# Optimization experiments

Hardware: AMD Instinct MI355X
Metric: run time of the kernel (lower is better)

Reference implementation:

```python
import jax, jax.numpy as jnp
import numpy as np

B, NQ, NK = 8, 1024, 1024
DQ = DK = DV = 512
H = 8
DH = DV // H
EPS = 1e-5
NEG = -1e9


def _layer_norm(x, g, b):
    mu = jnp.mean(x, axis=-1, keepdims=True)
    var = jnp.mean(jnp.square(x - mu), axis=-1, keepdims=True)
    return (x - mu) * jax.lax.rsqrt(var + EPS) * g + b


def setup_inputs() -> dict:
    key = jax.random.key(0)
    ks = jax.random.split(key, 16)
    s_q = 1.0 / np.sqrt(DQ)
    s_k = 1.0 / np.sqrt(DK)
    s_v = 1.0 / np.sqrt(DV)
    return {
        "Q": jax.random.normal(ks[0], (B, NQ, DQ), jnp.float32),
        "K": jax.random.normal(ks[1], (B, NK, DK), jnp.float32),
        "mask": jax.random.randint(ks[2], (B, NK), 0, 2, jnp.int32),
        "Wq": jax.random.uniform(ks[3], (DQ, DV), jnp.float32, -s_q, s_q),
        "bq": jax.random.uniform(ks[4], (DV,), jnp.float32, -s_q, s_q),
        "Wk": jax.random.uniform(ks[5], (DK, DV), jnp.float32, -s_k, s_k),
        "bk": jax.random.uniform(ks[6], (DV,), jnp.float32, -s_k, s_k),
        "Wv": jax.random.uniform(ks[7], (DK, DV), jnp.float32, -s_k, s_k),
        "bv": jax.random.uniform(ks[8], (DV,), jnp.float32, -s_k, s_k),
        "Wo": jax.random.uniform(ks[9], (DV, DV), jnp.float32, -s_v, s_v),
        "bo": jax.random.uniform(ks[10], (DV,), jnp.float32, -s_v, s_v),
        "g0": jnp.ones((DV,), jnp.float32),
        "b0": jnp.zeros((DV,), jnp.float32),
        "g1": jnp.ones((DV,), jnp.float32),
        "b1": jnp.zeros((DV,), jnp.float32),
    }


def reference(Q, K, mask, Wq, bq, Wk, bk, Wv, bv, Wo, bo, g0, b0, g1, b1):
    b = Q.shape[0]
    # projections: [B, N, DV] -> [B, N, H, DH]
    q = (Q @ Wq + bq).reshape(b, -1, H, DH)
    k = (K @ Wk + bk).reshape(b, -1, H, DH)
    v = (K @ Wv + bv).reshape(b, -1, H, DH)
    scores = jnp.einsum("bqhd,bkhd->bhqk", q, k) / np.sqrt(DH)  # [B,H,Nq,Nk]
    scores = jnp.where((mask == 0)[:, None, None, :], NEG, scores)
    A = jax.nn.softmax(scores, axis=-1)
    o = q + jnp.einsum("bhqk,bkhd->bqhd", A, v)  # residual on projected Q (per head)
    O = o.reshape(b, -1, DV)
    O = _layer_norm(O, g0, b0)
    O = O + jax.nn.relu(O @ Wo + bo)
    O = _layer_norm(O, g1, b1)
    return O
```

## Files before the change

### kernel.cpp

```cpp
#include <hip/hip_runtime.h>


typedef float f32x4 __attribute__((ext_vector_type(4)));
typedef short bf16x8 __attribute__((ext_vector_type(8)));
typedef unsigned short u16;

#define MFMA16 __builtin_amdgcn_mfma_f32_16x16x32_bf16

__device__ __forceinline__ float bf2f(u16 u){
    unsigned x = ((unsigned)u) << 16;
    return __builtin_bit_cast(float, x);
}
__device__ __forceinline__ u16 f2bf(float f){
    unsigned u = __builtin_bit_cast(unsigned, f);
    u = u + 0x7fffu + ((u >> 16) & 1u);
    return (u16)(u >> 16);
}

__global__ __launch_bounds__(256) void transpose_w(
    const float* __restrict__ Wq, const float* __restrict__ Wk,
    const float* __restrict__ Wv, const float* __restrict__ Wo,
    u16* __restrict__ wt)
{
    const int z = blockIdx.z;
    const float* W = (z == 0) ? Wq : (z == 1) ? Wk : (z == 2) ? Wv : Wo;
    u16* out = wt + (size_t)z * 512 * 512;

    __shared__ u16 tile[32][33];
    const int k0 = blockIdx.y * 32, n0 = blockIdx.x * 32;
    const int c = threadIdx.x & 31, r = threadIdx.x >> 5;
#pragma unroll
    for (int i = 0; i < 4; i++) {
        int rr = r + i * 8;
        tile[rr][c] = f2bf(W[(size_t)(k0 + rr) * 512 + n0 + c]);
    }
    __syncthreads();
#pragma unroll
    for (int i = 0; i < 4; i++) {
        int rr = r + i * 8;
        out[(size_t)(n0 + rr) * 512 + k0 + c] = tile[c][rr];
    }
}

__global__ __launch_bounds__(256) void transpose_v(
    const u16* __restrict__ vb, u16* __restrict__ vtg)
{
    __shared__ u16 tile[32][33];
    const int bh = blockIdx.z;
    const int b = bh >> 3, h = bh & 7;
    const int k0 = blockIdx.x * 32, d0 = blockIdx.y * 32;
    const int c = threadIdx.x & 31, r = threadIdx.x >> 5;
#pragma unroll
    for (int i = 0; i < 4; i++) {
        int rr = r + i * 8;
        tile[rr][c] = vb[(size_t)(b * 1024 + k0 + rr) * 512 + h * 64 + d0 + c];
    }
    __syncthreads();
#pragma unroll
    for (int i = 0; i < 4; i++) {
        int rr = r + i * 8;
        vtg[(size_t)(bh * 64 + d0 + rr) * 1024 + k0 + c] = tile[c][rr];
    }
}

__global__ __launch_bounds__(256) void gemm_proj(
    const float* __restrict__ Q, const float* __restrict__ K,
    const u16* __restrict__ wt,
    const float* __restrict__ bq, const float* __restrict__ bk, const float* __restrict__ bv,
    u16* __restrict__ qb, u16* __restrict__ kb, u16* __restrict__ vb)
{
    __shared__ __align__(16) u16 lds_a[128 * 40];
    __shared__ __align__(16) u16 lds_b[128 * 40];

    const int z = blockIdx.z;
    const float* X = (z == 0) ? Q : K;
    const u16* Wt = wt + (size_t)z * 512 * 512;
    const float* bias = (z == 0) ? bq : (z == 1) ? bk : bv;
    u16* outb = (z == 0) ? qb : (z == 1) ? kb : vb;

    const int bm = blockIdx.y, bn = blockIdx.x;
    const int t = threadIdx.x;
    const int wave = t >> 6, lane = t & 63, quad = lane >> 4, lm = lane & 15;
    const int wm = wave >> 1, wn = wave & 1;

    f32x4 acc[4][4];
    const f32x4 zz = {0.f, 0.f, 0.f, 0.f};
#pragma unroll
    for (int i = 0; i < 4; i++)
#pragma unroll
        for (int j = 0; j < 4; j++) acc[i][j] = zz;

    for (int k0 = 0; k0 < 512; k0 += 32) {
#pragma unroll
        for (int i = 0; i < 2; i++) {
            int idx = t + i * 256;
            int r = idx >> 2, c = (idx & 3) * 8;
            const float* xp = &X[(size_t)(bm * 128 + r) * 512 + k0 + c];
            f32x4 a0 = *(const f32x4*)xp;
            f32x4 a1 = *(const f32x4*)(xp + 4);
            bf16x8 xv;
#pragma unroll
            for (int j = 0; j < 4; j++) { xv[j] = (short)f2bf(a0[j]); xv[4 + j] = (short)f2bf(a1[j]); }
            *(bf16x8*)&lds_a[r * 40 + c] = xv;
            *(bf16x8*)&lds_b[r * 40 + c] =
                *(const bf16x8*)&Wt[(size_t)(bn * 128 + r) * 512 + k0 + c];
        }
        __syncthreads();
        bf16x8 af[4], bfr[4];
#pragma unroll
        for (int mi = 0; mi < 4; mi++)
            af[mi] = *(const bf16x8*)&lds_a[(wm * 64 + mi * 16 + lm) * 40 + quad * 8];
#pragma unroll
        for (int ni = 0; ni < 4; ni++)
            bfr[ni] = *(const bf16x8*)&lds_b[(wn * 64 + ni * 16 + lm) * 40 + quad * 8];
#pragma unroll
        for (int mi = 0; mi < 4; mi++)
#pragma unroll
            for (int ni = 0; ni < 4; ni++)
                acc[mi][ni] = MFMA16(af[mi], bfr[ni], acc[mi][ni], 0, 0, 0);
        __syncthreads();
    }

#pragma unroll
    for (int mi = 0; mi < 4; mi++) {
#pragma unroll
        for (int ni = 0; ni < 4; ni++) {
            const int col = bn * 128 + wn * 64 + ni * 16 + lm;
            const float bv_ = bias[col];
#pragma unroll
            for (int r = 0; r < 4; r++) {
                const int row = bm * 128 + wm * 64 + mi * 16 + quad * 4 + r;
                outb[(size_t)row * 512 + col] = f2bf(acc[mi][ni][r] + bv_);
            }
        }
    }
}

__global__ __launch_bounds__(256) void gemm_mlp(
    const u16* __restrict__ X, const u16* __restrict__ wt,
    const float* __restrict__ bo, const float* __restrict__ resid,
    float* __restrict__ outf)
{
    __shared__ __align__(16) u16 lds_a[128 * 40];
    __shared__ __align__(16) u16 lds_b[128 * 40];

    const u16* Wt = wt + (size_t)3 * 512 * 512;
    const int bm = blockIdx.y, bn = blockIdx.x;
    const int t = threadIdx.x;
    const int wave = t >> 6, lane = t & 63, quad = lane >> 4, lm = lane & 15;
    const int wm = wave >> 1, wn = wave & 1;

    f32x4 acc[4][4];
    const f32x4 zz = {0.f, 0.f, 0.f, 0.f};
#pragma unroll
    for (int i = 0; i < 4; i++)
#pragma unroll
        for (int j = 0; j < 4; j++) acc[i][j] = zz;

    for (int k0 = 0; k0 < 512; k0 += 32) {
#pragma unroll
        for (int i = 0; i < 2; i++) {
            int idx = t + i * 256;
            int r = idx >> 2, c = (idx & 3) * 8;
            *(bf16x8*)&lds_a[r * 40 + c] =
                *(const bf16x8*)&X[(size_t)(bm * 128 + r) * 512 + k0 + c];
            *(bf16x8*)&lds_b[r * 40 + c] =
                *(const bf16x8*)&Wt[(size_t)(bn * 128 + r) * 512 + k0 + c];
        }
        __syncthreads();
        bf16x8 af[4], bfr[4];
#pragma unroll
        for (int mi = 0; mi < 4; mi++)
            af[mi] = *(const bf16x8*)&lds_a[(wm * 64 + mi * 16 + lm) * 40 + quad * 8];
#pragma unroll
        for (int ni = 0; ni < 4; ni++)
            bfr[ni] = *(const bf16x8*)&lds_b[(wn * 64 + ni * 16 + lm) * 40 + quad * 8];
#pragma unroll
        for (int mi = 0; mi < 4; mi++)
#pragma unroll
            for (int ni = 0; ni < 4; ni++)
                acc[mi][ni] = MFMA16(af[mi], bfr[ni], acc[mi][ni], 0, 0, 0);
        __syncthreads();
    }

#pragma unroll
    for (int mi = 0; mi < 4; mi++) {
#pragma unroll
        for (int ni = 0; ni < 4; ni++) {
            const int col = bn * 128 + wn * 64 + ni * 16 + lm;
            const float bv_ = bo[col];
#pragma unroll
            for (int r = 0; r < 4; r++) {
                const int row = bm * 128 + wm * 64 + mi * 16 + quad * 4 + r;
                const size_t off = (size_t)row * 512 + col;
                outf[off] = resid[off] + fmaxf(acc[mi][ni][r] + bv_, 0.f);
            }
        }
    }
}

__global__ __launch_bounds__(256) void attn_kernel(
    const u16* __restrict__ qb, const u16* __restrict__ kb, const u16* __restrict__ vtg,
    const int* __restrict__ mask, float* __restrict__ O)
{
    __shared__ __align__(16) u16 k_tile[64 * 88];
    __shared__ __align__(16) u16 vt[64 * 88];
    __shared__ __align__(16) u16 p_st[4 * 32 * 88];
    __shared__ float mskf[1024];

    const int i = blockIdx.x;
    const int s_ = i >> 3;
    const int bh = (i & 7) + 8 * (s_ >> 3);
    const int qt = s_ & 7;
    const int b = bh >> 3, h = bh & 7;

    const int t = threadIdx.x, wave = t >> 6, lane = t & 63;
    const int quad = lane >> 4, lm = lane & 15;
    const int qbase = qt * 128 + wave * 32;
    const size_t baseb = (size_t)b * 1024 * 512;
    const size_t vbase = (size_t)((b * 8 + h) * 64) * 1024;

#pragma unroll
    for (int ii = 0; ii < 4; ii++) {
        int j = t + ii * 256;
        mskf[j] = mask[b * 1024 + j] ? 1.0f : 0.0f;
    }

    bf16x8 aq[2][2];
#pragma unroll
    for (int m = 0; m < 2; m++)
#pragma unroll
        for (int ks = 0; ks < 2; ks++)
            aq[m][ks] = *(const bf16x8*)&qb[baseb +
                (size_t)(qbase + m * 16 + lm) * 512 + h * 64 + ks * 32 + quad * 8];

    float lsum[2][4];
    f32x4 oacc[2][4];
    const f32x4 zz = {0.f, 0.f, 0.f, 0.f};
#pragma unroll
    for (int m = 0; m < 2; m++) {
#pragma unroll
        for (int r = 0; r < 4; r++) lsum[m][r] = 0.f;
#pragma unroll
        for (int c = 0; c < 4; c++) oacc[m][c] = zz;
    }

    const float SC2 = 0.125f * 1.44269504088896341f;
    const int srow = t >> 2, scol = (t & 3) * 16;
    u16* pw = &p_st[wave * 32 * 88];

    for (int kt = 0; kt < 16; ++kt) {
        const int keyg = kt * 64;
        {
            const u16* kp = &kb[baseb + (size_t)(keyg + srow) * 512 + h * 64 + scol];
            *(bf16x8*)&k_tile[srow * 88 + scol]     = *(const bf16x8*)kp;
            *(bf16x8*)&k_tile[srow * 88 + scol + 8] = *(const bf16x8*)(kp + 8);
            const u16* vp = &vtg[vbase + (size_t)srow * 1024 + keyg + scol];
            *(bf16x8*)&vt[srow * 88 + scol]     = *(const bf16x8*)vp;
            *(bf16x8*)&vt[srow * 88 + scol + 8] = *(const bf16x8*)(vp + 8);
        }
        __syncthreads();

        bf16x8 bk[4][2];
#pragma unroll
        for (int n = 0; n < 4; n++)
#pragma unroll
            for (int ks = 0; ks < 2; ks++)
                bk[n][ks] = *(const bf16x8*)&k_tile[(n * 16 + lm) * 88 + ks * 32 + quad * 8];

#pragma unroll
        for (int m = 0; m < 2; m++) {
#pragma unroll
            for (int n = 0; n < 4; n++) {
                f32x4 S = zz;
                S = MFMA16(aq[m][0], bk[n][0], S, 0, 0, 0);
                S = MFMA16(aq[m][1], bk[n][1], S, 0, 0, 0);
                const float mf = mskf[keyg + n * 16 + lm];
#pragma unroll
                for (int r = 0; r < 4; r++) {
                    float p = __builtin_amdgcn_exp2f(S[r] * SC2) * mf;
                    lsum[m][r] += p;
                    pw[(m * 16 + quad * 4 + r) * 88 + n * 16 + lm] = f2bf(p);
                }
            }
        }

#pragma unroll
        for (int m = 0; m < 2; m++) {
#pragma unroll
            for (int ks = 0; ks < 2; ks++) {
                bf16x8 ap = *(const bf16x8*)&pw[(m * 16 + lm) * 88 + ks * 32 + quad * 8];
#pragma unroll
                for (int c = 0; c < 4; c++) {
                    bf16x8 bv_ = *(const bf16x8*)&vt[(c * 16 + lm) * 88 + ks * 32 + quad * 8];
                    oacc[m][c] = MFMA16(ap, bv_, oacc[m][c], 0, 0, 0);
                }
            }
        }
        __syncthreads();
    }

#pragma unroll
    for (int m = 0; m < 2; m++)
#pragma unroll
        for (int r = 0; r < 4; r++) {
            float s = lsum[m][r];
            s += __shfl_xor(s, 1); s += __shfl_xor(s, 2);
            s += __shfl_xor(s, 4); s += __shfl_xor(s, 8);
            lsum[m][r] = s;
        }

#pragma unroll
    for (int m = 0; m < 2; m++)
#pragma unroll
        for (int c = 0; c < 4; c++)
#pragma unroll
            for (int r = 0; r < 4; r++) {
                const int row = qbase + m * 16 + quad * 4 + r;
                const int d = h * 64 + c * 16 + lm;
                const size_t off = baseb + (size_t)row * 512 + d;
                O[off] = bf2f(qb[off]) + oacc[m][c][r] / lsum[m][r];
            }
}

__global__ __launch_bounds__(256) void ln_kernel(
    const float* __restrict__ in, const float* __restrict__ g, const float* __restrict__ bsh,
    u16* __restrict__ outb, float* __restrict__ outf)
{
    const int row = blockIdx.x * 4 + (threadIdx.x >> 6);
    const int lane = threadIdx.x & 63;
    const float* x = in + (size_t)row * 512 + lane * 8;
    float v[8];
    *(f32x4*)&v[0] = *(const f32x4*)&x[0];
    *(f32x4*)&v[4] = *(const f32x4*)&x[4];
    float s = 0.f, sq = 0.f;
#pragma unroll
    for (int j = 0; j < 8; j++) { s += v[j]; sq += v[j] * v[j]; }
#pragma unroll
    for (int off = 1; off < 64; off <<= 1) {
        s += __shfl_xor(s, off);
        sq += __shfl_xor(sq, off);
    }
    const float mu = s * (1.f / 512.f);
    const float var = sq * (1.f / 512.f) - mu * mu;
    const float rs = rsqrtf(var + 1e-5f);
    float y[8];
#pragma unroll
    for (int j = 0; j < 8; j++) {
        int col = lane * 8 + j;
        y[j] = (v[j] - mu) * rs * g[col] + bsh[col];
    }
    if (outb != nullptr) {
        bf16x8 ov;
#pragma unroll
        for (int j = 0; j < 8; j++) ov[j] = (short)f2bf(y[j]);
        *(bf16x8*)&outb[(size_t)row * 512 + lane * 8] = ov;
    }
    if (outf != nullptr) {
        float* o = outf + (size_t)row * 512 + lane * 8;
        *(f32x4*)&o[0] = *(const f32x4*)&y[0];
        *(f32x4*)&o[4] = *(const f32x4*)&y[4];
    }
}

extern "C" void kernel_launch(void* const* d_in, const int* in_sizes, int n_in,
                              void* d_out, int out_size, void* d_ws, size_t ws_size,
                              hipStream_t stream) {
    const float* Q  = (const float*)d_in[0];
    const float* K  = (const float*)d_in[1];
    const int* mask = (const int*)d_in[2];
    const float* Wq = (const float*)d_in[3];
    const float* bq = (const float*)d_in[4];
    const float* Wk = (const float*)d_in[5];
    const float* bk = (const float*)d_in[6];
    const float* Wv = (const float*)d_in[7];
    const float* bv = (const float*)d_in[8];
    const float* Wo = (const float*)d_in[9];
    const float* bo = (const float*)d_in[10];
    const float* g0 = (const float*)d_in[11];
    const float* b0 = (const float*)d_in[12];
    const float* g1 = (const float*)d_in[13];
    const float* b1 = (const float*)d_in[14];
    float* out = (float*)d_out;

    char* ws = (char*)d_ws;
    const size_t MB = 1048576;
    u16*   wt  = (u16*)(ws);
    u16*   qb  = (u16*)(ws + 2 * MB);
    u16*   kb  = (u16*)(ws + 10 * MB);
    u16*   vtg = (u16*)(ws + 18 * MB);
    u16*   vb  = (u16*)(ws + 26 * MB);
    float* Of  = (float*)(ws + 26 * MB);
    u16*   O1b = (u16*)(ws + 2 * MB);
    float* O1f = (float*)(ws + 10 * MB);
    float* Uf  = (float*)(ws + 26 * MB);

    transpose_w<<<dim3(16, 16, 4), 256, 0, stream>>>(Wq, Wk, Wv, Wo, wt);
    gemm_proj<<<dim3(4, 64, 3), 256, 0, stream>>>(Q, K, wt, bq, bk, bv, qb, kb, vb);
    transpose_v<<<dim3(32, 2, 64), 256, 0, stream>>>(vb, vtg);
    attn_kernel<<<512, 256, 0, stream>>>(qb, kb, vtg, mask, Of);
    ln_kernel<<<2048, 256, 0, stream>>>(Of, g0, b0, O1b, O1f);
    gemm_mlp<<<dim3(4, 64, 1), 256, 0, stream>>>(O1b, wt, bo, O1f, Uf);
    ln_kernel<<<2048, 256, 0, stream>>>(Uf, g1, b1, nullptr, out);
}
```

Before: 208.5 us.

## Fuse V transpose into projection epilogue and merge LN-MLP-LN into one kernel

The V projection epilogue now writes directly in the per-head transposed layout that attention expects, so the separate transpose_v kernel and its round trip through memory go away. The two layernorm kernels and the MLP GEMM are replaced by a single kernel. Each block normalizes 32 rows into LDS as bf16, runs the GEMM against the full Wo, and does the residual, ReLU and second layernorm in registers with a cross-wave reduction. This removes three launches and the fp32 intermediate buffers. In exchange, each block re-reads the whole weight matrix, only 256 blocks run, and the residual now comes from the bf16 normalized values instead of fp32.

After: 210.7 us. Within noise of the previous version (+1.0%).

```diff
diff --git a/kernel.cpp b/kernel.cpp
--- a/kernel.cpp
+++ b/kernel.cpp
@@ -4,6 +4,7 @@
 typedef float f32x4 __attribute__((ext_vector_type(4)));
 typedef short bf16x8 __attribute__((ext_vector_type(8)));
 typedef unsigned short u16;
+typedef unsigned short u16x4 __attribute__((ext_vector_type(4)));
 
 #define MFMA16 __builtin_amdgcn_mfma_f32_16x16x32_bf16
 
@@ -42,32 +43,11 @@
     }
 }
 
-__global__ __launch_bounds__(256) void transpose_v(
-    const u16* __restrict__ vb, u16* __restrict__ vtg)
-{
-    __shared__ u16 tile[32][33];
-    const int bh = blockIdx.z;
-    const int b = bh >> 3, h = bh & 7;
-    const int k0 = blockIdx.x * 32, d0 = blockIdx.y * 32;
-    const int c = threadIdx.x & 31, r = threadIdx.x >> 5;
-#pragma unroll
-    for (int i = 0; i < 4; i++) {
-        int rr = r + i * 8;
-        tile[rr][c] = vb[(size_t)(b * 1024 + k0 + rr) * 512 + h * 64 + d0 + c];
-    }
-    __syncthreads();
-#pragma unroll
-    for (int i = 0; i < 4; i++) {
-        int rr = r + i * 8;
-        vtg[(size_t)(bh * 64 + d0 + rr) * 1024 + k0 + c] = tile[c][rr];
-    }
-}
-
 __global__ __launch_bounds__(256) void gemm_proj(
     const float* __restrict__ Q, const float* __restrict__ K,
     const u16* __restrict__ wt,
     const float* __restrict__ bq, const float* __restrict__ bk, const float* __restrict__ bv,
-    u16* __restrict__ qb, u16* __restrict__ kb, u16* __restrict__ vb)
+    u16* __restrict__ qb, u16* __restrict__ kb, u16* __restrict__ vtg)
 {
     __shared__ __align__(16) u16 lds_a[128 * 40];
     __shared__ __align__(16) u16 lds_b[128 * 40];
@@ -76,7 +56,6 @@
     const float* X = (z == 0) ? Q : K;
     const u16* Wt = wt + (size_t)z * 512 * 512;
     const float* bias = (z == 0) ? bq : (z == 1) ? bk : bv;
-    u16* outb = (z == 0) ? qb : (z == 1) ? kb : vb;
 
     const int bm = blockIdx.y, bn = blockIdx.x;
     const int t = threadIdx.x;
@@ -121,79 +100,36 @@
         __syncthreads();
     }
 
-#pragma unroll
-    for (int mi = 0; mi < 4; mi++) {
-#pragma unroll
-        for (int ni = 0; ni < 4; ni++) {
-            const int col = bn * 128 + wn * 64 + ni * 16 + lm;
-            const float bv_ = bias[col];
-#pragma unroll
-            for (int r = 0; r < 4; r++) {
-                const int row = bm * 128 + wm * 64 + mi * 16 + quad * 4 + r;
-                outb[(size_t)row * 512 + col] = f2bf(acc[mi][ni][r] + bv_);
-            }
-        }
-    }
-}
-
-__global__ __launch_bounds__(256) void gemm_mlp(
-    const u16* __restrict__ X, const u16* __restrict__ wt,
-    const float* __restrict__ bo, const float* __restrict__ resid,
-    float* __restrict__ outf)
-{
-    __shared__ __align__(16) u16 lds_a[128 * 40];
-    __shared__ __align__(16) u16 lds_b[128 * 40];
-
-    const u16* Wt = wt + (size_t)3 * 512 * 512;
-    const int bm = blockIdx.y, bn = blockIdx.x;
-    const int t = threadIdx.x;
-    const int wave = t >> 6, lane = t & 63, quad = lane >> 4, lm = lane & 15;
-    const int wm = wave >> 1, wn = wave & 1;
-
-    f32x4 acc[4][4];
-    const f32x4 zz = {0.f, 0.f, 0.f, 0.f};
-#pragma unroll
-    for (int i = 0; i < 4; i++)
-#pragma unroll
-        for (int j = 0; j < 4; j++) acc[i][j] = zz;
-
-    for (int k0 = 0; k0 < 512; k0 += 32) {
-#pragma unroll
-        for (int i = 0; i < 2; i++) {
-            int idx = t + i * 256;
-            int r = idx >> 2, c = (idx & 3) * 8;
-            *(bf16x8*)&lds_a[r * 40 + c] =
-                *(const bf16x8*)&X[(size_t)(bm * 128 + r) * 512 + k0 + c];
-            *(bf16x8*)&lds_b[r * 40 + c] =
-                *(const bf16x8*)&Wt[(size_t)(bn * 128 + r) * 512 + k0 + c];
-        }
-        __syncthreads();
-        bf16x8 af[4], bfr[4];
-#pragma unroll
-        for (int mi = 0; mi < 4; mi++)
-            af[mi] = *(const bf16x8*)&lds_a[(wm * 64 + mi * 16 + lm) * 40 + quad * 8];
-#pragma unroll
-        for (int ni = 0; ni < 4; ni++)
-            bfr[ni] = *(const bf16x8*)&lds_b[(wn * 64 + ni * 16 + lm) * 40 + quad * 8];
-#pragma unroll
-        for (int mi = 0; mi < 4; mi++)
-#pragma unroll
-            for (int ni = 0; ni < 4; ni++)
-                acc[mi][ni] = MFMA16(af[mi], bfr[ni], acc[mi][ni], 0, 0, 0);
-        __syncthreads();
-    }
-
-#pragma unroll
-    for (int mi = 0; mi < 4; mi++) {
-#pragma unroll
-        for (int ni = 0; ni < 4; ni++) {
-            const int col = bn * 128 + wn * 64 + ni * 16 + lm;
-            const float bv_ = bo[col];
-#pragma unroll
-            for (int r = 0; r < 4; r++) {
-                const int row = bm * 128 + wm * 64 + mi * 16 + quad * 4 + r;
-                const size_t off = (size_t)row * 512 + col;
-                outf[off] = resid[off] + fmaxf(acc[mi][ni][r] + bv_, 0.f);
+    if (z < 2) {
+        u16* outb = (z == 0) ? qb : kb;
+#pragma unroll
+        for (int mi = 0; mi < 4; mi++) {
+#pragma unroll
+            for (int ni = 0; ni < 4; ni++) {
+                const int col = bn * 128 + wn * 64 + ni * 16 + lm;
+                const float bv_ = bias[col];
+#pragma unroll
+                for (int r = 0; r < 4; r++) {
+                    const int row = bm * 128 + wm * 64 + mi * 16 + quad * 4 + r;
+                    outb[(size_t)row * 512 + col] = f2bf(acc[mi][ni][r] + bv_);
+                }
+            }
+        }
+    } else {
+        const int b = bm >> 3;
+        const int key0 = (bm & 7) * 128 + wm * 64;
+#pragma unroll
+        for (int mi = 0; mi < 4; mi++) {
+#pragma unroll
+            for (int ni = 0; ni < 4; ni++) {
+                const int col = bn * 128 + wn * 64 + ni * 16 + lm;
+                const float bv_ = bias[col];
+                const int h = col >> 6, d = col & 63;
+                const int key = key0 + mi * 16 + quad * 4;
+                u16x4 pk;
+#pragma unroll
+                for (int r = 0; r < 4; r++) pk[r] = f2bf(acc[mi][ni][r] + bv_);
+                *(u16x4*)&vtg[(size_t)((b * 8 + h) * 64 + d) * 1024 + key] = pk;
             }
         }
     }
@@ -323,43 +259,155 @@
             }
 }
 
-__global__ __launch_bounds__(256) void ln_kernel(
-    const float* __restrict__ in, const float* __restrict__ g, const float* __restrict__ bsh,
-    u16* __restrict__ outb, float* __restrict__ outf)
+__global__ __launch_bounds__(256) void mega_mlp(
+    const float* __restrict__ Of, const u16* __restrict__ wt,
+    const float* __restrict__ bo,
+    const float* __restrict__ g0, const float* __restrict__ b0,
+    const float* __restrict__ g1, const float* __restrict__ b1,
+    float* __restrict__ out)
 {
-    const int row = blockIdx.x * 4 + (threadIdx.x >> 6);
-    const int lane = threadIdx.x & 63;
-    const float* x = in + (size_t)row * 512 + lane * 8;
-    float v[8];
-    *(f32x4*)&v[0] = *(const f32x4*)&x[0];
-    *(f32x4*)&v[4] = *(const f32x4*)&x[4];
-    float s = 0.f, sq = 0.f;
-#pragma unroll
-    for (int j = 0; j < 8; j++) { s += v[j]; sq += v[j] * v[j]; }
-#pragma unroll
-    for (int off = 1; off < 64; off <<= 1) {
-        s += __shfl_xor(s, off);
-        sq += __shfl_xor(sq, off);
-    }
-    const float mu = s * (1.f / 512.f);
-    const float var = sq * (1.f / 512.f) - mu * mu;
-    const float rs = rsqrtf(var + 1e-5f);
-    float y[8];
-#pragma unroll
-    for (int j = 0; j < 8; j++) {
-        int col = lane * 8 + j;
-        y[j] = (v[j] - mu) * rs * g[col] + bsh[col];
-    }
-    if (outb != nullptr) {
-        bf16x8 ov;
-#pragma unroll
-        for (int j = 0; j < 8; j++) ov[j] = (short)f2bf(y[j]);
-        *(bf16x8*)&outb[(size_t)row * 512 + lane * 8] = ov;
-    }
-    if (outf != nullptr) {
-        float* o = outf + (size_t)row * 512 + lane * 8;
-        *(f32x4*)&o[0] = *(const f32x4*)&y[0];
-        *(f32x4*)&o[4] = *(const f32x4*)&y[4];
+    __shared__ __align__(16) u16 lnA[32 * 536];
+    __shared__ __align__(16) u16 Bs[512 * 40];
+    __shared__ float ws_s[4][32];
+    __shared__ float ws_q[4][32];
+
+    const u16* Wt = wt + (size_t)3 * 512 * 512;
+    const int bm = blockIdx.x;
+    const int t = threadIdx.x, wave = t >> 6, lane = t & 63;
+    const int quad = lane >> 4, lm = lane & 15;
+    const size_t rowbase = (size_t)bm * 32;
+
+    {
+        const int r = t >> 3, c0 = (t & 7) * 64;
+        const float* x = &Of[(rowbase + r) * 512 + c0];
+        float v[64];
+#pragma unroll
+        for (int j = 0; j < 16; j++) *(f32x4*)&v[j * 4] = *(const f32x4*)&x[j * 4];
+        float s = 0.f, sq = 0.f;
+#pragma unroll
+        for (int j = 0; j < 64; j++) { s += v[j]; sq += v[j] * v[j]; }
+        s += __shfl_xor(s, 1); sq += __shfl_xor(sq, 1);
+        s += __shfl_xor(s, 2); sq += __shfl_xor(sq, 2);
+        s += __shfl_xor(s, 4); sq += __shfl_xor(sq, 4);
+        const float mu = s * (1.f / 512.f);
+        const float var = sq * (1.f / 512.f) - mu * mu;
+        const float rs = rsqrtf(var + 1e-5f);
+#pragma unroll
+        for (int j0 = 0; j0 < 64; j0 += 8) {
+            bf16x8 ov;
+#pragma unroll
+            for (int j = 0; j < 8; j++) {
+                const int col = c0 + j0 + j;
+                ov[j] = (short)f2bf((v[j0 + j] - mu) * rs * g0[col] + b0[col]);
+            }
+            *(bf16x8*)&lnA[r * 536 + c0 + j0] = ov;
+        }
+    }
+    __syncthreads();
+
+    f32x4 acc[2][8];
+    const f32x4 zz = {0.f, 0.f, 0.f, 0.f};
+#pragma unroll
+    for (int mi = 0; mi < 2; mi++)
+#pragma unroll
+        for (int ni = 0; ni < 8; ni++) acc[mi][ni] = zz;
+
+    for (int k0 = 0; k0 < 512; k0 += 32) {
+#pragma unroll
+        for (int i = 0; i < 8; i++) {
+            int idx = t + i * 256;
+            int row = idx >> 2, kc = (idx & 3) * 8;
+            *(bf16x8*)&Bs[row * 40 + kc] =
+                *(const bf16x8*)&Wt[(size_t)row * 512 + k0 + kc];
+        }
+        __syncthreads();
+        bf16x8 af[2], bfr[8];
+#pragma unroll
+        for (int mi = 0; mi < 2; mi++)
+            af[mi] = *(const bf16x8*)&lnA[(mi * 16 + lm) * 536 + k0 + quad * 8];
+#pragma unroll
+        for (int ni = 0; ni < 8; ni++)
+            bfr[ni] = *(const bf16x8*)&Bs[(wave * 128 + ni * 16 + lm) * 40 + quad * 8];
+#pragma unroll
+        for (int mi = 0; mi < 2; mi++)
+#pragma unroll
+            for (int ni = 0; ni < 8; ni++)
+                acc[mi][ni] = MFMA16(af[mi], bfr[ni], acc[mi][ni], 0, 0, 0);
+        __syncthreads();
+    }
+
+    float ps[2][4], pq[2][4];
+#pragma unroll
+    for (int mi = 0; mi < 2; mi++)
+#pragma unroll
+        for (int r = 0; r < 4; r++) { ps[mi][r] = 0.f; pq[mi][r] = 0.f; }
+
+#pragma unroll
+    for (int ni = 0; ni < 8; ni++) {
+        const int col = wave * 128 + ni * 16 + lm;
+        const float bov = bo[col];
+#pragma unroll
+        for (int mi = 0; mi < 2; mi++) {
+#pragma unroll
+            for (int r = 0; r < 4; r++) {
+                const int row = mi * 16 + quad * 4 + r;
+                const float resid = bf2f(lnA[row * 536 + col]);
+                const float yy = resid + fmaxf(acc[mi][ni][r] + bov, 0.f);
+                acc[mi][ni][r] = yy;
+                ps[mi][r] += yy;
+                pq[mi][r] += yy * yy;
+            }
+        }
+    }
+#pragma unroll
+    for (int mi = 0; mi < 2; mi++)
+#pragma unroll
+        for (int r = 0; r < 4; r++) {
+            float s = ps[mi][r], q = pq[mi][r];
+            s += __shfl_xor(s, 1); q += __shfl_xor(q, 1);
+            s += __shfl_xor(s, 2); q += __shfl_xor(q, 2);
+            s += __shfl_xor(s, 4); q += __shfl_xor(q, 4);
+            s += __shfl_xor(s, 8); q += __shfl_xor(q, 8);
+            ps[mi][r] = s; pq[mi][r] = q;
+        }
+    if (lm == 0) {
+#pragma unroll
+        for (int mi = 0; mi < 2; mi++)
+#pragma unroll
+            for (int r = 0; r < 4; r++) {
+                const int row = mi * 16 + quad * 4 + r;
+                ws_s[wave][row] = ps[mi][r];
+                ws_q[wave][row] = pq[mi][r];
+            }
+    }
+    __syncthreads();
+
+    float murow[2][4], rsrow[2][4];
+#pragma unroll
+    for (int mi = 0; mi < 2; mi++)
+#pragma unroll
+        for (int r = 0; r < 4; r++) {
+            const int row = mi * 16 + quad * 4 + r;
+            const float S = ws_s[0][row] + ws_s[1][row] + ws_s[2][row] + ws_s[3][row];
+            const float Q2 = ws_q[0][row] + ws_q[1][row] + ws_q[2][row] + ws_q[3][row];
+            const float mu = S * (1.f / 512.f);
+            const float var = Q2 * (1.f / 512.f) - mu * mu;
+            murow[mi][r] = mu;
+            rsrow[mi][r] = rsqrtf(var + 1e-5f);
+        }
+
+#pragma unroll
+    for (int ni = 0; ni < 8; ni++) {
+        const int col = wave * 128 + ni * 16 + lm;
+        const float g1v = g1[col], b1v = b1[col];
+#pragma unroll
+        for (int mi = 0; mi < 2; mi++)
+#pragma unroll
+            for (int r = 0; r < 4; r++) {
+                const int row = mi * 16 + quad * 4 + r;
+                out[(rowbase + row) * 512 + col] =
+                    (acc[mi][ni][r] - murow[mi][r]) * rsrow[mi][r] * g1v + b1v;
+            }
     }
 }
 
@@ -389,17 +437,10 @@
     u16*   qb  = (u16*)(ws + 2 * MB);
     u16*   kb  = (u16*)(ws + 10 * MB);
     u16*   vtg = (u16*)(ws + 18 * MB);
-    u16*   vb  = (u16*)(ws + 26 * MB);
     float* Of  = (float*)(ws + 26 * MB);
-    u16*   O1b = (u16*)(ws + 2 * MB);
-    float* O1f = (float*)(ws + 10 * MB);
-    float* Uf  = (float*)(ws + 26 * MB);
 
     transpose_w<<<dim3(16, 16, 4), 256, 0, stream>>>(Wq, Wk, Wv, Wo, wt);
-    gemm_proj<<<dim3(4, 64, 3), 256, 0, stream>>>(Q, K, wt, bq, bk, bv, qb, kb, vb);
-    transpose_v<<<dim3(32, 2, 64), 256, 0, stream>>>(vb, vtg);
+    gemm_proj<<<dim3(4, 64, 3), 256, 0, stream>>>(Q, K, wt, bq, bk, bv, qb, kb, vtg);
     attn_kernel<<<512, 256, 0, stream>>>(qb, kb, vtg, mask, Of);
-    ln_kernel<<<2048, 256, 0, stream>>>(Of, g0, b0, O1b, O1f);
-    gemm_mlp<<<dim3(4, 64, 1), 256, 0, stream>>>(O1b, wt, bo, O1f, Uf);
-    ln_kernel<<<2048, 256, 0, stream>>>(Uf, g1, b1, nullptr, out);
-}
+    mega_mlp<<<256, 256, 0, stream>>>(Of, wt, bo, g0, b0, g1, b1, out);
+}
```
